# Kernel optimization log

Measured on AMD Instinct MI355X. Metric: run time of the kernel, lower is better.

## Reference

```python
import jax, jax.numpy as jnp
import numpy as np

N = 20000       # nodes
E = 320000      # edges (before self-loops)
F_IN = 1024     # num_features
H = 4           # head_num
C = 64          # hidden_size
NC = 4          # n_classes
NEG_SLOPE = 0.2 # PyG GATConv default


def setup_inputs() -> dict:
    key = jax.random.key(0)
    ks = jax.random.split(key, 16)
    def w(k, shape, fan_in):
        return jax.random.normal(k, shape, dtype=jnp.float32) / np.sqrt(fan_in)
    x = jax.random.normal(ks[0], (N, F_IN), dtype=jnp.float32)
    edge_index = jax.random.randint(ks[1], (2, E), 0, N, dtype=jnp.int64)
    return {
        "x": x,
        "edge_index": edge_index,
        # layer 1: F_IN -> H*C, concat
        "w1": w(ks[2], (F_IN, H * C), F_IN),
        "as1": w(ks[3], (H, C), C),
        "ad1": w(ks[4], (H, C), C),
        "b1": jnp.zeros((H * C,), jnp.float32),
        # layer 2: H*C -> H*C, concat
        "w2": w(ks[5], (H * C, H * C), H * C),
        "as2": w(ks[6], (H, C), C),
        "ad2": w(ks[7], (H, C), C),
        "b2": jnp.zeros((H * C,), jnp.float32),
        # out layer: H*C -> C, 1 head, concat=False
        "w3": w(ks[8], (H * C, 1 * C), H * C),
        "as3": w(ks[9], (1, C), C),
        "ad3": w(ks[10], (1, C), C),
        "b3": jnp.zeros((C,), jnp.float32),
        # classifier
        "wc": w(ks[11], (C, NC), C),
        "bc": jnp.zeros((NC,), jnp.float32),
    }


def gat_layer(x, src, dst, W, a_src, a_dst, bias, concat):
    """PyG GATConv (eval mode, self-loops already added to src/dst)."""
    n = x.shape[0]
    Hh, Cc = a_src.shape
    h = (x @ W).reshape(n, Hh, Cc)                       # [N,H,C]
    al_s = jnp.sum(h * a_src[None], axis=-1)             # [N,H]
    al_d = jnp.sum(h * a_dst[None], axis=-1)             # [N,H]
    e = al_s[src] + al_d[dst]                            # [E,H]
    e = jax.nn.leaky_relu(e, NEG_SLOPE)
    # segment softmax over incoming edges of each destination node
    emax = jax.ops.segment_max(e, dst, num_segments=n)   # [N,H]
    ex = jnp.exp(e - emax[dst])
    denom = jax.ops.segment_sum(ex, dst, num_segments=n) # [N,H]
    alpha = ex / (denom[dst] + 1e-16)                    # [E,H]
    msg = h[src] * alpha[..., None]                      # [E,H,C]
    out = jax.ops.segment_sum(msg, dst, num_segments=n)  # [N,H,C]
    if concat:
        out = out.reshape(n, Hh * Cc)
    else:
        out = out.mean(axis=1)
    return out + bias


def reference(x, edge_index, w1, as1, ad1, b1, w2, as2, ad2, b2,
              w3, as3, ad3, b3, wc, bc):
    n = x.shape[0]
    loop = jnp.arange(n, dtype=edge_index.dtype)
    src = jnp.concatenate([edge_index[0], loop])
    dst = jnp.concatenate([edge_index[1], loop])
    out = jax.nn.relu(gat_layer(x, src, dst, w1, as1, ad1, b1, True))
    out = jax.nn.relu(gat_layer(out, src, dst, w2, as2, ad2, b2, True))
    out = gat_layer(out, src, dst, w3, as3, ad3, b3, False)
    return out @ wc + bc                                  # [N, n_classes]
```

## Files before the change

### kernel.cpp

```cpp
#include <hip/hip_runtime.h>

#define N_NODES 20000
#define N_EDGES 320000
#define ET (N_EDGES + N_NODES)
#define F_IN 1024
#define HC 256
#define NC 4

typedef unsigned short ushort_t;
typedef __attribute__((ext_vector_type(8))) short short8;
typedef __attribute__((ext_vector_type(4))) float f32x4;

__device__ inline ushort_t f2bf(float f) {
    unsigned u = __float_as_uint(f);
    unsigned r = (u + 0x7fffu + ((u >> 16) & 1u)) >> 16;
    return (ushort_t)r;
}
__device__ inline float bf2f(ushort_t u) {
    return __uint_as_float(((unsigned)u) << 16);
}

__device__ inline unsigned cvt_pk_bf16(float lo, float hi) {
    unsigned r;
    asm("v_cvt_pk_bf16_f32 %0, %1, %2" : "=v"(r) : "v"(lo), "v"(hi));
    return r;
}

#define GLOAD16(gp, lp) __builtin_amdgcn_global_load_lds( \
    (const __attribute__((address_space(1))) void*)(gp),  \
    (__attribute__((address_space(3))) void*)(lp), 16, 0, 0)

__global__ void count_kernel(const int* __restrict__ ei, int* __restrict__ counts) {
    int e = blockIdx.x * blockDim.x + threadIdx.x;
    if (e >= ET) return;
    int dst = (e < N_EDGES) ? ei[N_EDGES + e] : (e - N_EDGES);
    atomicAdd(&counts[dst], 1);
}

__global__ void scan_kernel(const int* __restrict__ counts, int* __restrict__ row_ptr,
                            int* __restrict__ cursor) {
    __shared__ int sums[1024];
    int t = threadIdx.x;
    const int per = (N_NODES + 1023) / 1024;
    int b = t * per;
    int e = min(b + per, N_NODES);
    int s = 0;
    for (int i = b; i < e; ++i) s += counts[i];
    sums[t] = s;
    __syncthreads();
    for (int off = 1; off < 1024; off <<= 1) {
        int v = (t >= off) ? sums[t - off] : 0;
        __syncthreads();
        sums[t] += v;
        __syncthreads();
    }
    int run = (t == 0) ? 0 : sums[t - 1];
    for (int i = b; i < e; ++i) {
        row_ptr[i] = run;
        cursor[i]  = run;
        run += counts[i];
    }
    if (t == 0) row_ptr[N_NODES] = ET;
}

__global__ void scatter_kernel(const int* __restrict__ ei, int* __restrict__ cursor,
                               int* __restrict__ col) {
    int e = blockIdx.x * blockDim.x + threadIdx.x;
    if (e >= ET) return;
    int src, dst;
    if (e < N_EDGES) { src = ei[e]; dst = ei[N_EDGES + e]; }
    else             { src = dst = e - N_EDGES; }
    int pos = atomicAdd(&cursor[dst], 1);
    col[pos] = src;
}

__global__ void split_T(const float* __restrict__ in, ushort_t* __restrict__ hi,
                        ushort_t* __restrict__ lo, int K, int Nn) {
    int idx = blockIdx.x * blockDim.x + threadIdx.x;
    if (idx >= K * Nn) return;
    int k = idx / Nn, n = idx - k * Nn;
    float v = in[idx];
    ushort_t h = f2bf(v);
    hi[(size_t)n * K + k] = h;
    lo[(size_t)n * K + k] = f2bf(v - bf2f(h));
}

#define AL_EPILOGUE()                                                              \
    {                                                                              \
        float asv[NF], adv[NF];                                                    \
        _Pragma("unroll")                                                          \
        for (int j = 0; j < NF; ++j) {                                             \
            int col = bn + wn * SN + j * 16 + (lane & 15);                         \
            asv[j] = as_w[col];                                                    \
            adv[j] = ad_w[col];                                                    \
        }                                                                          \
        float* s_as = (float*)smem;                                   \
        float* s_ad = (float*)smem + 2 * BM;                                       \
        _Pragma("unroll")                                                          \
        for (int i = 0; i < MF; ++i) {                                             \
            _Pragma("unroll")                                                      \
            for (int rr = 0; rr < 4; ++rr) {                                       \
                float ps = 0.f, pd = 0.f;                                          \
                _Pragma("unroll")                                                  \
                for (int j = 0; j < NF; ++j) {                                     \
                    ps += acc[i][j][rr] * asv[j];                                  \
                    pd += acc[i][j][rr] * adv[j];                                  \
                }                                                                  \
                _Pragma("unroll")                                                  \
                for (int o = 1; o < 16; o <<= 1) {                                 \
                    ps += __shfl_xor(ps, o, 64);                                   \
                    pd += __shfl_xor(pd, o, 64);                                   \
                }                                                                  \
                if ((lane & 15) == 0) {                                            \
                    int rl = wm * SM + i * 16 + (lane >> 4) * 4 + rr;              \
                    s_as[wn * BM + rl] = ps;                                       \
                    s_ad[wn * BM + rl] = pd;                                       \
                }                                                                  \
            }                                                                      \
        }                                                                          \
        __syncthreads();                                                           \
        if (t < BM) {                                                              \
            int row = bm + t;                                                      \
            if (row < M) {                                                         \
                int hb = bn >> 6;                                                  \
                als[row * H + hb] = s_as[t] + s_as[BM + t];                        \
                ald[row * H + hb] = s_ad[t] + s_ad[BM + t];                        \
            }                                                                      \
        }                                                                          \
    }

template<int GY>
__launch_bounds__(256)
__global__ void gemm_f32a_ks(const float* __restrict__ X,
                             const ushort_t* __restrict__ BTh, const ushort_t* __restrict__ BTl,
                             float* __restrict__ Cp0, float* __restrict__ Cp1,
                             int M, int K, int NT) {
    constexpr int BM = 128, BN = 64, SM = 64, SN = 32, MF = 4, NF = 2;
    __shared__ __align__(16) char smem[24576];

    const int t = threadIdx.x, lane = t & 63, w = t >> 6;
    const int wm = w >> 1, wn = w & 1;
    const int nwg = gridDim.x;
    const int id = blockIdx.x;
    const int q = nwg >> 3, r = nwg & 7;
    const int xcd = id & 7, idx = id >> 3;
    const int logical = (xcd < r ? xcd * (q + 1) : r * (q + 1) + (xcd - r) * q) + idx;
    const int nwg_half = nwg >> 1;
    const int ks = logical / nwg_half;
    const int rem = logical - ks * nwg_half;
    const int bm = (rem / GY) * BM, bn = (rem % GY) * BN;
    const int kbase = ks * (K >> 1);
    float* Cp = ks ? Cp1 : Cp0;

    const int achk = lane & 3;
    const float* xRow[2]; int aoff[2];
    #pragma unroll
    for (int qq = 0; qq < 2; ++qq) {
        int arow = (w * 2 + qq) * 16 + (lane >> 2);
        int grow = min(bm + arow, M - 1);
        xRow[qq] = X + (size_t)grow * K + kbase + achk * 8;
        aoff[qq] = arow * 64 + ((achk ^ ((arow >> 1) & 3)) * 16);
    }
    const int gchunk = ((lane & 3) ^ ((lane >> 3) & 3)) * 16;
    const int brow = w * 16 + (lane >> 2);
    const size_t gB = (size_t)(bn + brow) * K * 2 + (size_t)kbase * 2 + gchunk;
    const int lB = w * 1024;

    const char* Bhb = (const char*)BTh;
    const char* Blb = (const char*)BTl;
    const int c16 = (lane >> 4);
    const int NTs = K >> 6;

    f32x4 acc[MF][NF];
    #pragma unroll
    for (int i = 0; i < MF; ++i)
        #pragma unroll
        for (int j = 0; j < NF; ++j) acc[i][j] = (f32x4){0.f, 0.f, 0.f, 0.f};

    float4 cur0[2], cur1[2], nxt0[2], nxt1[2];
    #pragma unroll
    for (int qq = 0; qq < 2; ++qq) {
        cur0[qq] = *(const float4*)(xRow[qq]);
        cur1[qq] = *(const float4*)(xRow[qq] + 4);
    }

    for (int ts = 0; ts < NTs; ++ts) {
        size_t kb = (size_t)ts * 64;
        GLOAD16(Bhb + gB + kb, smem + 16384 + lB);
        GLOAD16(Blb + gB + kb, smem + 20480 + lB);
        #pragma unroll
        for (int qq = 0; qq < 2; ++qq) {
            float vv[8] = {cur0[qq].x, cur0[qq].y, cur0[qq].z, cur0[qq].w,
                           cur1[qq].x, cur1[qq].y, cur1[qq].z, cur1[qq].w};
            unsigned hp[4], lp[4];
            #pragma unroll
            for (int j = 0; j < 4; ++j) {
                unsigned h = cvt_pk_bf16(vv[2 * j], vv[2 * j + 1]);
                float h0 = __uint_as_float(h << 16);
                float h1 = __uint_as_float(h & 0xFFFF0000u);
                hp[j] = h;
                lp[j] = cvt_pk_bf16(vv[2 * j] - h0, vv[2 * j + 1] - h1);
            }
            *(uint4*)(smem + aoff[qq])        = make_uint4(hp[0], hp[1], hp[2], hp[3]);
            *(uint4*)(smem + 8192 + aoff[qq]) = make_uint4(lp[0], lp[1], lp[2], lp[3]);
        }
        __syncthreads();
        if (ts + 1 < NTs) {
            int ko = (ts + 1) * 32;
            #pragma unroll
            for (int qq = 0; qq < 2; ++qq) {
                nxt0[qq] = *(const float4*)(xRow[qq] + ko);
                nxt1[qq] = *(const float4*)(xRow[qq] + ko + 4);
            }
        }
        short8 afh[MF], afl[MF], bfh[NF], bfl[NF];
        #pragma unroll
        for (int i = 0; i < MF; ++i) {
            int row = wm * SM + i * 16 + (lane & 15);
            int off = row * 64 + ((c16 ^ ((row >> 1) & 3)) * 16);
            afh[i] = *(const short8*)(smem + off);
            afl[i] = *(const short8*)(smem + 8192 + off);
        }
        #pragma unroll
        for (int j = 0; j < NF; ++j) {
            int row = wn * SN + j * 16 + (lane & 15);
            int off = row * 64 + ((c16 ^ ((row >> 1) & 3)) * 16);
            bfh[j] = *(const short8*)(smem + 16384 + off);
            bfl[j] = *(const short8*)(smem + 20480 + off);
        }
        #pragma unroll
        for (int i = 0; i < MF; ++i)
            #pragma unroll
            for (int j = 0; j < NF; ++j) {
                acc[i][j] = __builtin_amdgcn_mfma_f32_16x16x32_bf16(afh[i], bfh[j], acc[i][j], 0, 0, 0);
                acc[i][j] = __builtin_amdgcn_mfma_f32_16x16x32_bf16(afh[i], bfl[j], acc[i][j], 0, 0, 0);
                acc[i][j] = __builtin_amdgcn_mfma_f32_16x16x32_bf16(afl[i], bfh[j], acc[i][j], 0, 0, 0);
            }
        __syncthreads();
        #pragma unroll
        for (int qq = 0; qq < 2; ++qq) { cur0[qq] = nxt0[qq]; cur1[qq] = nxt1[qq]; }
    }
    #pragma unroll
    for (int i = 0; i < MF; ++i) {
        int rbase = bm + wm * SM + i * 16 + (lane >> 4) * 4;
        #pragma unroll
        for (int j = 0; j < NF; ++j) {
            int col = bn + wn * SN + j * 16 + (lane & 15);
            #pragma unroll
            for (int rr = 0; rr < 4; ++rr)
                if (rbase + rr < M) Cp[(size_t)(rbase + rr) * NT + col] = acc[i][j][rr];
        }
    }
}

__launch_bounds__(256)
__global__ void reduce_al(float* __restrict__ B0, const float* __restrict__ Cp1,
                          const float* __restrict__ as_w, const float* __restrict__ ad_w,
                          float* __restrict__ als, float* __restrict__ ald) {
    int lane = threadIdx.x & 63, w = threadIdx.x >> 6;
    int row = blockIdx.x * 4 + w;
    if (row >= N_NODES) return;
    size_t base = (size_t)row * HC + lane * 4;
    float4 p0 = *(const float4*)&B0[base];
    float4 p1 = *(const float4*)&Cp1[base];
    float4 s = make_float4(p0.x + p1.x, p0.y + p1.y, p0.z + p1.z, p0.w + p1.w);
    *(float4*)&B0[base] = s;
    int head = lane >> 4;
    int cw = (lane & 15) * 4;
    float ps = s.x * as_w[head * 64 + cw + 0] + s.y * as_w[head * 64 + cw + 1]
             + s.z * as_w[head * 64 + cw + 2] + s.w * as_w[head * 64 + cw + 3];
    float pd = s.x * ad_w[head * 64 + cw + 0] + s.y * ad_w[head * 64 + cw + 1]
             + s.z * ad_w[head * 64 + cw + 2] + s.w * ad_w[head * 64 + cw + 3];
    #pragma unroll
    for (int o = 1; o < 16; o <<= 1) {
        ps += __shfl_xor(ps, o, 64);
        pd += __shfl_xor(pd, o, 64);
    }
    if ((lane & 15) == 0) {
        als[row * 4 + head] = ps;
        ald[row * 4 + head] = pd;
    }
}

template<int BMT, int GY, int H>
__launch_bounds__(256)
__global__ void gemm_mfma(const ushort_t* __restrict__ Ah, const ushort_t* __restrict__ Al,
                          const ushort_t* __restrict__ BTh, const ushort_t* __restrict__ BTl,
                          float* __restrict__ C, const float* __restrict__ as_w,
                          const float* __restrict__ ad_w, float* __restrict__ als,
                          float* __restrict__ ald, int M, int K, int NT) {
    constexpr int BM = BMT, BN = 64, SM = BM / 2, SN = 32, MF = SM / 16, NF = 2;
    constexpr int AQ = BM / 64;
    constexpr int ASZ = BM * 64;
    __shared__ __align__(16) char smem[4 * ASZ + 16384];

    const int t = threadIdx.x, lane = t & 63, w = t >> 6;
    const int wm = w >> 1, wn = w & 1;
    const int nwg = gridDim.x;
    const int id = blockIdx.x;
    const int q = nwg >> 3, r = nwg & 7;
    const int xcd = id & 7, idx = id >> 3;
    const int logical = (xcd < r ? xcd * (q + 1) : r * (q + 1) + (xcd - r) * q) + idx;
    const int bm = (logical / GY) * BM, bn = (logical % GY) * BN;
    const int gchunk = ((lane & 3) ^ ((lane >> 3) & 3)) * 16;

    size_t gA[AQ]; int lA[AQ];
    #pragma unroll
    for (int qq = 0; qq < AQ; ++qq) {
        int inst = w * AQ + qq;
        int arow = inst * 16 + (lane >> 2);
        int grow = min(bm + arow, M - 1);
        gA[qq] = (size_t)grow * K * 2 + gchunk;
        lA[qq] = inst * 1024;
    }
    const int brow = w * 16 + (lane >> 2);
    const size_t gB = (size_t)(bn + brow) * K * 2 + gchunk;
    const int lB = w * 1024;

    const char* Ahb = (const char*)Ah;
    const char* Alb = (const char*)Al;
    const char* Bhb = (const char*)BTh;
    const char* Blb = (const char*)BTl;
    const int c16 = (lane >> 4);
    const int NTs = K / 64;

    f32x4 acc[MF][NF];
    #pragma unroll
    for (int i = 0; i < MF; ++i)
        #pragma unroll
        for (int j = 0; j < NF; ++j) acc[i][j] = (f32x4){0.f, 0.f, 0.f, 0.f};

    for (int ts = 0; ts < NTs; ++ts) {
        size_t kb = (size_t)ts * 128;
        #pragma unroll
        for (int kc = 0; kc < 2; ++kc) {
            #pragma unroll
            for (int qq = 0; qq < AQ; ++qq) {
                GLOAD16(Ahb + gA[qq] + kb + kc * 64, smem + kc * ASZ + lA[qq]);
                GLOAD16(Alb + gA[qq] + kb + kc * 64, smem + 2 * ASZ + kc * ASZ + lA[qq]);
            }
            GLOAD16(Bhb + gB + kb + kc * 64, smem + 4 * ASZ + kc * 4096 + lB);
            GLOAD16(Blb + gB + kb + kc * 64, smem + 4 * ASZ + 8192 + kc * 4096 + lB);
        }
        __syncthreads();
        #pragma unroll
        for (int kc = 0; kc < 2; ++kc) {
            short8 afh[MF], afl[MF], bfh[NF], bfl[NF];
            #pragma unroll
            for (int i = 0; i < MF; ++i) {
                int row = wm * SM + i * 16 + (lane & 15);
                int off = row * 64 + ((c16 ^ ((row >> 1) & 3)) * 16);
                afh[i] = *(const short8*)(smem + kc * ASZ + off);
                afl[i] = *(const short8*)(smem + 2 * ASZ + kc * ASZ + off);
            }
            #pragma unroll
            for (int j = 0; j < NF; ++j) {
                int row = wn * SN + j * 16 + (lane & 15);
                int off = row * 64 + ((c16 ^ ((row >> 1) & 3)) * 16);
                bfh[j] = *(const short8*)(smem + 4 * ASZ + kc * 4096 + off);
                bfl[j] = *(const short8*)(smem + 4 * ASZ + 8192 + kc * 4096 + off);
            }
            #pragma unroll
            for (int i = 0; i < MF; ++i)
                #pragma unroll
                for (int j = 0; j < NF; ++j) {
                    acc[i][j] = __builtin_amdgcn_mfma_f32_16x16x32_bf16(afh[i], bfh[j], acc[i][j], 0, 0, 0);
                    acc[i][j] = __builtin_amdgcn_mfma_f32_16x16x32_bf16(afh[i], bfl[j], acc[i][j], 0, 0, 0);
                    acc[i][j] = __builtin_amdgcn_mfma_f32_16x16x32_bf16(afl[i], bfh[j], acc[i][j], 0, 0, 0);
                }
        }
        __syncthreads();
    }
    #pragma unroll
    for (int i = 0; i < MF; ++i) {
        int rbase = bm + wm * SM + i * 16 + (lane >> 4) * 4;
        #pragma unroll
        for (int j = 0; j < NF; ++j) {
            int col = bn + wn * SN + j * 16 + (lane & 15);
            #pragma unroll
            for (int rr = 0; rr < 4; ++rr)
                if (rbase + rr < M) C[(size_t)(rbase + rr) * NT + col] = acc[i][j][rr];
        }
    }
    AL_EPILOGUE()
}

template<int CT, int CW, int H, bool RELU, bool SPLIT, bool CLS>
__launch_bounds__(256)
__global__ void agg_v6(const float* __restrict__ h, const float* __restrict__ als,
                       const float* __restrict__ ald,
                       const int* __restrict__ row_ptr, const int* __restrict__ col,
                       const float* __restrict__ bias,
                       ushort_t* __restrict__ oh, ushort_t* __restrict__ ol,
                       float* __restrict__ of,
                       const float* __restrict__ wc, const float* __restrict__ bc,
                       float* __restrict__ cls_out) {
    constexpr int NS  = CT / CW;
    constexpr int LPT = CW / 4;
    constexpr int TPW = 64 / LPT;
    static_assert(NS == H, "slice==head mapping");
    __shared__ int   s_src[4][64];
    __shared__ float s_alp[4][64];
    const int nwg = gridDim.x;
    const int q = nwg >> 3;
    int id = blockIdx.x;
    int logical = (id & 7) * q + (id >> 3);
    int slice = logical / (N_NODES / 4);
    int g = logical - slice * (N_NODES / 4);
    int lane = threadIdx.x & 63, w = threadIdx.x >> 6;
    int dst = g * 4 + w;
    int beg = row_ptr[dst], deg = row_ptr[dst + 1] - beg;
    int team = lane / LPT;
    int cc = (lane & (LPT - 1)) * 4;

    const int*   colP = col + beg;
    const float* hS   = h + slice * CW + cc;
    float ad = ald[dst * H + slice];

    float m = -1e30f, den = 0.f;
    for (int base = 0; base < deg; base += 64) {
        int i = base + lane;
        if (i < deg) {
            float e = als[colP[i] * H + slice] + ad;
            e = (e > 0.f) ? e : 0.2f * e;
            float nm = fmaxf(m, e);
            den = den * __expf(m - nm) + __expf(e - nm);
            m = nm;
        }
    }
    #pragma unroll
    for (int off = 1; off < 64; off <<= 1) {
        float mo = __shfl_xor(m, off, 64);
        float dn = __shfl_xor(den, off, 64);
        float nm = fmaxf(m, mo);
        den = den * __expf(m - nm) + dn * __expf(mo - nm);
        m = nm;
    }
    float rden = 1.f / (den + 1e-16f);

    float4 a0v = make_float4(0.f, 0.f, 0.f, 0.f);
    float4 a1v = make_float4(0.f, 0.f, 0.f, 0.f);
    float4 a2v = make_float4(0.f, 0.f, 0.f, 0.f);
    float4 a3v = make_float4(0.f, 0.f, 0.f, 0.f);
    for (int base = 0; base < deg; base += 64) {
        int cnt = min(64, deg - base);
        if (lane < cnt) {
            int src = colP[base + lane];
            s_src[w][lane] = src;
            float e = als[src * H + slice] + ad;
            e = (e > 0.f) ? e : 0.2f * e;
            s_alp[w][lane] = __expf(e - m) * rden;
        }
        int i = team;
        for (; i + 3 * TPW < cnt; i += 4 * TPW) {
            int   s0 = s_src[w][i],           s1 = s_src[w][i + TPW];
            int   s2 = s_src[w][i + 2 * TPW], s3 = s_src[w][i + 3 * TPW];
            float a0 = s_alp[w][i],           a1 = s_alp[w][i + TPW];
            float a2 = s_alp[w][i + 2 * TPW], a3 = s_alp[w][i + 3 * TPW];
            float4 h0 = *(const float4*)&hS[s0 * CT];
            float4 h1 = *(const float4*)&hS[s1 * CT];
            float4 h2 = *(const float4*)&hS[s2 * CT];
            float4 h3 = *(const float4*)&hS[s3 * CT];
            a0v.x += a0 * h0.x; a0v.y += a0 * h0.y; a0v.z += a0 * h0.z; a0v.w += a0 * h0.w;
            a1v.x += a1 * h1.x; a1v.y += a1 * h1.y; a1v.z += a1 * h1.z; a1v.w += a1 * h1.w;
            a2v.x += a2 * h2.x; a2v.y += a2 * h2.y; a2v.z += a2 * h2.z; a2v.w += a2 * h2.w;
            a3v.x += a3 * h3.x; a3v.y += a3 * h3.y; a3v.z += a3 * h3.z; a3v.w += a3 * h3.w;
        }
        for (; i < cnt; i += TPW) {
            int   s0 = s_src[w][i];
            float a0 = s_alp[w][i];
            float4 h0 = *(const float4*)&hS[s0 * CT];
            a0v.x += a0 * h0.x; a0v.y += a0 * h0.y; a0v.z += a0 * h0.z; a0v.w += a0 * h0.w;
        }
    }
    float4 acc = make_float4((a0v.x + a1v.x) + (a2v.x + a3v.x),
                             (a0v.y + a1v.y) + (a2v.y + a3v.y),
                             (a0v.z + a1v.z) + (a2v.z + a3v.z),
                             (a0v.w + a1v.w) + (a2v.w + a3v.w));
    #pragma unroll
    for (int off = LPT; off < 64; off <<= 1) {
        acc.x += __shfl_xor(acc.x, off, 64);
        acc.y += __shfl_xor(acc.y, off, 64);
        acc.z += __shfl_xor(acc.z, off, 64);
        acc.w += __shfl_xor(acc.w, off, 64);
    }
    if (team == 0) {
        int ch = slice * CW + cc;
        float4 bv = *(const float4*)&bias[ch];
        float v0 = acc.x + bv.x, v1 = acc.y + bv.y, v2 = acc.z + bv.z, v3 = acc.w + bv.w;
        if (RELU) {
            v0 = fmaxf(v0, 0.f); v1 = fmaxf(v1, 0.f);
            v2 = fmaxf(v2, 0.f); v3 = fmaxf(v3, 0.f);
        }
        if (CLS) {
            float ps[NC];
            #pragma unroll
            for (int k = 0; k < NC; ++k)
                ps[k] = v0 * wc[(cc + 0) * NC + k] + v1 * wc[(cc + 1) * NC + k]
                      + v2 * wc[(cc + 2) * NC + k] + v3 * wc[(cc + 3) * NC + k];
            #pragma unroll
            for (int o = 1; o < 16; o <<= 1)
                #pragma unroll
                for (int k = 0; k < NC; ++k) ps[k] += __shfl_xor(ps[k], o, 64);
            if (lane == 0) {
                #pragma unroll
                for (int k = 0; k < NC; ++k) cls_out[(size_t)dst * NC + k] = ps[k] + bc[k];
            }
        } else {
            size_t idx = (size_t)dst * CT + ch;
            if (SPLIT) {
                ushort4 h4, l4;
                h4.x = f2bf(v0); l4.x = f2bf(v0 - bf2f(h4.x));
                h4.y = f2bf(v1); l4.y = f2bf(v1 - bf2f(h4.y));
                h4.z = f2bf(v2); l4.z = f2bf(v2 - bf2f(h4.z));
                h4.w = f2bf(v3); l4.w = f2bf(v3 - bf2f(h4.w));
                *(ushort4*)&oh[idx] = h4;
                *(ushort4*)&ol[idx] = l4;
            } else {
                *(float4*)&of[idx] = make_float4(v0, v1, v2, v3);
            }
        }
    }
}

extern "C" void kernel_launch(void* const* d_in, const int* in_sizes, int n_in,
                              void* d_out, int out_size, void* d_ws, size_t ws_size,
                              hipStream_t stream) {
    const float* x   = (const float*)d_in[0];
    const int*   ei  = (const int*)d_in[1];
    const float* w1  = (const float*)d_in[2];
    const float* as1 = (const float*)d_in[3];
    const float* ad1 = (const float*)d_in[4];
    const float* b1  = (const float*)d_in[5];
    const float* w2  = (const float*)d_in[6];
    const float* as2 = (const float*)d_in[7];
    const float* ad2 = (const float*)d_in[8];
    const float* b2  = (const float*)d_in[9];
    const float* w3  = (const float*)d_in[10];
    const float* as3 = (const float*)d_in[11];
    const float* ad3 = (const float*)d_in[12];
    const float* b3  = (const float*)d_in[13];
    const float* wc  = (const float*)d_in[14];
    const float* bc  = (const float*)d_in[15];
    float* out = (float*)d_out;

    char* ws = (char*)d_ws;
    size_t off = 0;
    auto alloc = [&](size_t bytes) -> char* {
        char* p = ws + off;
        off = (off + bytes + 255) & ~(size_t)255;
        return p;
    };

    int* counts  = (int*)alloc(N_NODES * 4);
    int* cursor  = (int*)alloc(N_NODES * 4);
    int* row_ptr = (int*)alloc((N_NODES + 1) * 4);
    int* colidx  = (int*)alloc(ET * 4);
    float* als   = (float*)alloc(N_NODES * 4 * 4);
    float* ald   = (float*)alloc(N_NODES * 4 * 4);
    float* B0    = (float*)alloc((size_t)N_NODES * HC * 4);
    float* Cp1   = (float*)alloc((size_t)N_NODES * HC * 4);

    ushort_t* w1Th = (ushort_t*)alloc((size_t)F_IN * HC * 2);
    ushort_t* w1Tl = (ushort_t*)alloc((size_t)F_IN * HC * 2);
    ushort_t* w2Th = (ushort_t*)alloc((size_t)HC * HC * 2);
    ushort_t* w2Tl = (ushort_t*)alloc((size_t)HC * HC * 2);
    ushort_t* w3Th = (ushort_t*)alloc((size_t)HC * 64 * 2);
    ushort_t* w3Tl = (ushort_t*)alloc((size_t)HC * 64 * 2);
    ushort_t* B1h  = (ushort_t*)alloc((size_t)N_NODES * HC * 2);
    ushort_t* B1l  = (ushort_t*)alloc((size_t)N_NODES * HC * 2);

    hipMemsetAsync(counts, 0, N_NODES * sizeof(int), stream);
    int eb = (ET + 255) / 256;
    count_kernel<<<eb, 256, 0, stream>>>(ei, counts);
    scan_kernel<<<1, 1024, 0, stream>>>(counts, row_ptr, cursor);
    scatter_kernel<<<eb, 256, 0, stream>>>(ei, cursor, colidx);

    split_T<<<(F_IN * HC + 255) / 256, 256, 0, stream>>>(w1, w1Th, w1Tl, F_IN, HC);
    split_T<<<(HC * HC + 255) / 256, 256, 0, stream>>>(w2, w2Th, w2Tl, HC, HC);
    split_T<<<(HC * 64 + 255) / 256, 256, 0, stream>>>(w3, w3Th, w3Tl, HC, 64);

    const int nwg128 = ((N_NODES + 127) / 128) * (HC / 64);
    const int nblk_dst = N_NODES / 4;
    gemm_f32a_ks<4><<<2 * nwg128, 256, 0, stream>>>(x, w1Th, w1Tl, B0, Cp1, N_NODES, F_IN, HC);
    reduce_al<<<nblk_dst, 256, 0, stream>>>(B0, Cp1, as1, ad1, als, ald);
    agg_v6<256, 64, 4, true, true, false><<<4 * nblk_dst, 256, 0, stream>>>(
        B0, als, ald, row_ptr, colidx, b1, B1h, B1l, nullptr, nullptr, nullptr, nullptr);
    gemm_mfma<128, 4, 4><<<nwg128, 256, 0, stream>>>(B1h, B1l, w2Th, w2Tl, B0, as2, ad2,
                                                     als, ald, N_NODES, HC, HC);
    agg_v6<256, 64, 4, true, true, false><<<4 * nblk_dst, 256, 0, stream>>>(
        B0, als, ald, row_ptr, colidx, b2, B1h, B1l, nullptr, nullptr, nullptr, nullptr);
    const int nwg3 = (N_NODES + 63) / 64;
    gemm_mfma<64, 1, 1><<<nwg3, 256, 0, stream>>>(B1h, B1l, w3Th, w3Tl, B0, as3, ad3,
                                                  als, ald, N_NODES, HC, 64);
    agg_v6<64, 64, 1, false, false, true><<<nblk_dst, 256, 0, stream>>>(
        B0, als, ald, row_ptr, colidx, b3, nullptr, nullptr, nullptr, wc, bc, out);
}
```

Baseline: 288.8 us.

## Stage fp32 X tiles into LDS via direct loads and fuse prep kernels

```diff
diff --git a/kernel.cpp b/kernel.cpp
--- a/kernel.cpp
+++ b/kernel.cpp
@@ -30,11 +30,45 @@
     (const __attribute__((address_space(1))) void*)(gp),  \
     (__attribute__((address_space(3))) void*)(lp), 16, 0, 0)
 
-__global__ void count_kernel(const int* __restrict__ ei, int* __restrict__ counts) {
-    int e = blockIdx.x * blockDim.x + threadIdx.x;
-    if (e >= ET) return;
-    int dst = (e < N_EDGES) ? ei[N_EDGES + e] : (e - N_EDGES);
-    atomicAdd(&counts[dst], 1);
+__global__ void prep_kernel(const int* __restrict__ ei, int* __restrict__ counts,
+                            const float* __restrict__ w1, ushort_t* __restrict__ w1Th,
+                            ushort_t* __restrict__ w1Tl,
+                            const float* __restrict__ w2, ushort_t* __restrict__ w2Th,
+                            ushort_t* __restrict__ w2Tl,
+                            const float* __restrict__ w3, ushort_t* __restrict__ w3Th,
+                            ushort_t* __restrict__ w3Tl) {
+    const int EB = (ET + 255) / 256;
+    const int S1 = F_IN * HC / 256;
+    const int S2 = HC * HC / 256;
+    int b = blockIdx.x;
+    if (b < EB) {
+        int e = b * 256 + threadIdx.x;
+        if (e < ET) {
+            int dst = (e < N_EDGES) ? ei[N_EDGES + e] : (e - N_EDGES);
+            atomicAdd(&counts[dst], 1);
+        }
+    } else if (b < EB + S1) {
+        int idx = (b - EB) * 256 + threadIdx.x;
+        int k = idx / HC, n = idx - k * HC;
+        float v = w1[idx];
+        ushort_t h = f2bf(v);
+        w1Th[(size_t)n * F_IN + k] = h;
+        w1Tl[(size_t)n * F_IN + k] = f2bf(v - bf2f(h));
+    } else if (b < EB + S1 + S2) {
+        int idx = (b - EB - S1) * 256 + threadIdx.x;
+        int k = idx / HC, n = idx - k * HC;
+        float v = w2[idx];
+        ushort_t h = f2bf(v);
+        w2Th[(size_t)n * HC + k] = h;
+        w2Tl[(size_t)n * HC + k] = f2bf(v - bf2f(h));
+    } else {
+        int idx = (b - EB - S1 - S2) * 256 + threadIdx.x;
+        int k = idx / 64, n = idx - k * 64;
+        float v = w3[idx];
+        ushort_t h = f2bf(v);
+        w3Th[(size_t)n * HC + k] = h;
+        w3Tl[(size_t)n * HC + k] = f2bf(v - bf2f(h));
+    }
 }
 
 __global__ void scan_kernel(const int* __restrict__ counts, int* __restrict__ row_ptr,
@@ -72,17 +106,6 @@
     else             { src = dst = e - N_EDGES; }
     int pos = atomicAdd(&cursor[dst], 1);
     col[pos] = src;
-}
-
-__global__ void split_T(const float* __restrict__ in, ushort_t* __restrict__ hi,
-                        ushort_t* __restrict__ lo, int K, int Nn) {
-    int idx = blockIdx.x * blockDim.x + threadIdx.x;
-    if (idx >= K * Nn) return;
-    int k = idx / Nn, n = idx - k * Nn;
-    float v = in[idx];
-    ushort_t h = f2bf(v);
-    hi[(size_t)n * K + k] = h;
-    lo[(size_t)n * K + k] = f2bf(v - bf2f(h));
 }
 
 #define AL_EPILOGUE()                                                              \
@@ -136,7 +159,7 @@
                              float* __restrict__ Cp0, float* __restrict__ Cp1,
                              int M, int K, int NT) {
     constexpr int BM = 128, BN = 64, SM = 64, SN = 32, MF = 4, NF = 2;
-    __shared__ __align__(16) char smem[24576];
+    __shared__ __align__(16) char smem[49152];
 
     const int t = threadIdx.x, lane = t & 63, w = t >> 6;
     const int wm = w >> 1, wn = w & 1;
@@ -152,24 +175,25 @@
     const int kbase = ks * (K >> 1);
     float* Cp = ks ? Cp1 : Cp0;
 
-    const int achk = lane & 3;
-    const float* xRow[2]; int aoff[2];
-    #pragma unroll
-    for (int qq = 0; qq < 2; ++qq) {
-        int arow = (w * 2 + qq) * 16 + (lane >> 2);
-        int grow = min(bm + arow, M - 1);
-        xRow[qq] = X + (size_t)grow * K + kbase + achk * 8;
-        aoff[qq] = arow * 64 + ((achk ^ ((arow >> 1) & 3)) * 16);
+    size_t gA[4]; int lA[4];
+    #pragma unroll
+    for (int qq = 0; qq < 4; ++qq) {
+        int row  = (w * 4 + qq) * 8 + (lane >> 3);
+        int grow = min(bm + row, M - 1);
+        int sw16 = ((((lane >> 1) & 3) ^ (row & 3)) << 1) | (lane & 1);
+        gA[qq] = ((size_t)grow * K + kbase) * 4 + sw16 * 16;
+        lA[qq] = (w * 4 + qq) * 1024;
     }
     const int gchunk = ((lane & 3) ^ ((lane >> 3) & 3)) * 16;
     const int brow = w * 16 + (lane >> 2);
     const size_t gB = (size_t)(bn + brow) * K * 2 + (size_t)kbase * 2 + gchunk;
     const int lB = w * 1024;
 
+    const char* Xb  = (const char*)X;
     const char* Bhb = (const char*)BTh;
     const char* Blb = (const char*)BTl;
     const int c16 = (lane >> 4);
-    const int NTs = K >> 6;
+    const int NTs = K >> 7;
 
     f32x4 acc[MF][NF];
     #pragma unroll
@@ -177,68 +201,61 @@
         #pragma unroll
         for (int j = 0; j < NF; ++j) acc[i][j] = (f32x4){0.f, 0.f, 0.f, 0.f};
 
-    float4 cur0[2], cur1[2], nxt0[2], nxt1[2];
-    #pragma unroll
-    for (int qq = 0; qq < 2; ++qq) {
-        cur0[qq] = *(const float4*)(xRow[qq]);
-        cur1[qq] = *(const float4*)(xRow[qq] + 4);
-    }
-
     for (int ts = 0; ts < NTs; ++ts) {
-        size_t kb = (size_t)ts * 64;
-        GLOAD16(Bhb + gB + kb, smem + 16384 + lB);
-        GLOAD16(Blb + gB + kb, smem + 20480 + lB);
-        #pragma unroll
-        for (int qq = 0; qq < 2; ++qq) {
-            float vv[8] = {cur0[qq].x, cur0[qq].y, cur0[qq].z, cur0[qq].w,
-                           cur1[qq].x, cur1[qq].y, cur1[qq].z, cur1[qq].w};
-            unsigned hp[4], lp[4];
-            #pragma unroll
-            for (int j = 0; j < 4; ++j) {
-                unsigned h = cvt_pk_bf16(vv[2 * j], vv[2 * j + 1]);
-                float h0 = __uint_as_float(h << 16);
-                float h1 = __uint_as_float(h & 0xFFFF0000u);
-                hp[j] = h;
-                lp[j] = cvt_pk_bf16(vv[2 * j] - h0, vv[2 * j + 1] - h1);
+        size_t kbB = (size_t)ts * 128;
+        size_t kbA = (size_t)ts * 256;
+        #pragma unroll
+        for (int kc = 0; kc < 2; ++kc) {
+            #pragma unroll
+            for (int qq = 0; qq < 4; ++qq)
+                GLOAD16(Xb + gA[qq] + kbA + kc * 128, smem + kc * 16384 + lA[qq]);
+            GLOAD16(Bhb + gB + kbB + kc * 64, smem + 32768 + kc * 4096 + lB);
+            GLOAD16(Blb + gB + kbB + kc * 64, smem + 40960 + kc * 4096 + lB);
+        }
+        __syncthreads();
+        #pragma unroll
+        for (int kc = 0; kc < 2; ++kc) {
+            short8 afh[MF], afl[MF], bfh[NF], bfl[NF];
+            #pragma unroll
+            for (int i = 0; i < MF; ++i) {
+                int row = wm * SM + i * 16 + (lane & 15);
+                int off = kc * 16384 + row * 128 + ((c16 ^ (row & 3)) * 32);
+                float4 a0 = *(const float4*)(smem + off);
+                float4 a1 = *(const float4*)(smem + off + 16);
+                unsigned h0 = cvt_pk_bf16(a0.x, a0.y);
+                unsigned h1 = cvt_pk_bf16(a0.z, a0.w);
+                unsigned h2 = cvt_pk_bf16(a1.x, a1.y);
+                unsigned h3 = cvt_pk_bf16(a1.z, a1.w);
+                unsigned l0 = cvt_pk_bf16(a0.x - __uint_as_float(h0 << 16),
+                                          a0.y - __uint_as_float(h0 & 0xFFFF0000u));
+                unsigned l1 = cvt_pk_bf16(a0.z - __uint_as_float(h1 << 16),
+                                          a0.w - __uint_as_float(h1 & 0xFFFF0000u));
+                unsigned l2 = cvt_pk_bf16(a1.x - __uint_as_float(h2 << 16),
+                                          a1.y - __uint_as_float(h2 & 0xFFFF0000u));
+                unsigned l3 = cvt_pk_bf16(a1.z - __uint_as_float(h3 << 16),
+                                          a1.w - __uint_as_float(h3 & 0xFFFF0000u));
+                uint4 hv = make_uint4(h0, h1, h2, h3);
+                uint4 lv = make_uint4(l0, l1, l2, l3);
+                afh[i] = *(short8*)&hv;
+                afl[i] = *(short8*)&lv;
             }
-            *(uint4*)(smem + aoff[qq])        = make_uint4(hp[0], hp[1], hp[2], hp[3]);
-            *(uint4*)(smem + 8192 + aoff[qq]) = make_uint4(lp[0], lp[1], lp[2], lp[3]);
+            #pragma unroll
+            for (int j = 0; j < NF; ++j) {
+                int row = wn * SN + j * 16 + (lane & 15);
+                int off = row * 64 + ((c16 ^ ((row >> 1) & 3)) * 16);
+                bfh[j] = *(const short8*)(smem + 32768 + kc * 4096 + off);
+                bfl[j] = *(const short8*)(smem + 40960 + kc * 4096 + off);
+            }
+            #pragma unroll
+            for (int i = 0; i < MF; ++i)
+                #pragma unroll
+                for (int j = 0; j < NF; ++j) {
+                    acc[i][j] = __builtin_amdgcn_mfma_f32_16x16x32_bf16(afh[i], bfh[j], acc[i][j], 0, 0, 0);
+                    acc[i][j] = __builtin_amdgcn_mfma_f32_16x16x32_bf16(afh[i], bfl[j], acc[i][j], 0, 0, 0);
+                    acc[i][j] = __builtin_amdgcn_mfma_f32_16x16x32_bf16(afl[i], bfh[j], acc[i][j], 0, 0, 0);
+                }
         }
         __syncthreads();
-        if (ts + 1 < NTs) {
-            int ko = (ts + 1) * 32;
-            #pragma unroll
-            for (int qq = 0; qq < 2; ++qq) {
-                nxt0[qq] = *(const float4*)(xRow[qq] + ko);
-                nxt1[qq] = *(const float4*)(xRow[qq] + ko + 4);
-            }
-        }
-        short8 afh[MF], afl[MF], bfh[NF], bfl[NF];
-        #pragma unroll
-        for (int i = 0; i < MF; ++i) {
-            int row = wm * SM + i * 16 + (lane & 15);
-            int off = row * 64 + ((c16 ^ ((row >> 1) & 3)) * 16);
-            afh[i] = *(const short8*)(smem + off);
-            afl[i] = *(const short8*)(smem + 8192 + off);
-        }
-        #pragma unroll
-        for (int j = 0; j < NF; ++j) {
-            int row = wn * SN + j * 16 + (lane & 15);
-            int off = row * 64 + ((c16 ^ ((row >> 1) & 3)) * 16);
-            bfh[j] = *(const short8*)(smem + 16384 + off);
-            bfl[j] = *(const short8*)(smem + 20480 + off);
-        }
-        #pragma unroll
-        for (int i = 0; i < MF; ++i)
-            #pragma unroll
-            for (int j = 0; j < NF; ++j) {
-                acc[i][j] = __builtin_amdgcn_mfma_f32_16x16x32_bf16(afh[i], bfh[j], acc[i][j], 0, 0, 0);
-                acc[i][j] = __builtin_amdgcn_mfma_f32_16x16x32_bf16(afh[i], bfl[j], acc[i][j], 0, 0, 0);
-                acc[i][j] = __builtin_amdgcn_mfma_f32_16x16x32_bf16(afl[i], bfh[j], acc[i][j], 0, 0, 0);
-            }
-        __syncthreads();
-        #pragma unroll
-        for (int qq = 0; qq < 2; ++qq) { cur0[qq] = nxt0[qq]; cur1[qq] = nxt1[qq]; }
     }
     #pragma unroll
     for (int i = 0; i < MF; ++i) {
@@ -571,14 +588,12 @@
     ushort_t* B1l  = (ushort_t*)alloc((size_t)N_NODES * HC * 2);
 
     hipMemsetAsync(counts, 0, N_NODES * sizeof(int), stream);
-    int eb = (ET + 255) / 256;
-    count_kernel<<<eb, 256, 0, stream>>>(ei, counts);
+    const int EB = (ET + 255) / 256;
+    const int PREP = EB + F_IN * HC / 256 + HC * HC / 256 + HC * 64 / 256;
+    prep_kernel<<<PREP, 256, 0, stream>>>(ei, counts, w1, w1Th, w1Tl,
+                                          w2, w2Th, w2Tl, w3, w3Th, w3Tl);
     scan_kernel<<<1, 1024, 0, stream>>>(counts, row_ptr, cursor);
-    scatter_kernel<<<eb, 256, 0, stream>>>(ei, cursor, colidx);
-
-    split_T<<<(F_IN * HC + 255) / 256, 256, 0, stream>>>(w1, w1Th, w1Tl, F_IN, HC);
-    split_T<<<(HC * HC + 255) / 256, 256, 0, stream>>>(w2, w2Th, w2Tl, HC, HC);
-    split_T<<<(HC * 64 + 255) / 256, 256, 0, stream>>>(w3, w3Th, w3Tl, HC, 64);
+    scatter_kernel<<<EB, 256, 0, stream>>>(ei, cursor, colidx);
 
     const int nwg128 = ((N_NODES + 127) / 128) * (HC / 64);
     const int nblk_dst = N_NODES / 4;
```

Result: no change. 287.6 us (-0.4%).
